# Optimization experiments

Hardware: AMD Instinct MI355X
Metric: run time of the kernel (lower is better)

## Reference

```python
import jax, jax.numpy as jnp
import numpy as np

N_LOW = 50000
N_HIGH = 200000
E = 1000000       # number of (i, j, k) triplets from the radius search
K = 27            # 3x3x3 voxel kernel cells
C_IN = 128
C_OUT = 128


def setup_inputs() -> dict:
    key = jax.random.key(0)
    k0, k1, k2, k3, k4, k5 = jax.random.split(key, 6)
    x_low = jax.random.normal(k0, (N_LOW, C_IN), dtype=jnp.float32)
    # PointConv3d weight: one [C_OUT, C_IN] matrix per kernel cell, kaiming-ish scale
    weight = jax.random.normal(k1, (K, C_OUT, C_IN), dtype=jnp.float32) * (1.0 / np.sqrt(C_IN))
    bias = jax.random.normal(k2, (C_OUT,), dtype=jnp.float32) * 0.01
    i_high = jax.random.randint(k3, (E,), 0, N_HIGH, dtype=jnp.int32)
    j_low = jax.random.randint(k4, (E,), 0, N_LOW, dtype=jnp.int32)
    k_cell = jax.random.randint(k5, (E,), 0, K, dtype=jnp.int32)
    return {"x_low": x_low, "weight": weight, "bias": bias,
            "i_high": i_high, "j_low": j_low, "k": k_cell, "n_high": N_HIGH}


def reference(x_low, weight, bias, i_high, j_low, k, n_high):
    # Sparse point convolution: out[i] += weight[k] @ x_low[j], then + bias.
    # Efficient form: transform every low-res point by all K kernel matrices once
    # (dense GEMM), then gather the (j, k) entry per triplet and scatter-add by i.
    y = jnp.einsum('nc,koc->nko', x_low, weight)       # [N_low, K, C_out]
    msg = y[j_low, k]                                  # [E, C_out] gather
    out = jnp.zeros((n_high, weight.shape[1]), dtype=x_low.dtype)
    out = out.at[i_high].add(msg)                      # scatter-add to high-res points
    return out + bias
```

## Files before the change

kernel.cpp:

```cpp
#include <hip/hip_runtime.h>

typedef _Float16 half8 __attribute__((ext_vector_type(8)));
typedef _Float16 half4v __attribute__((ext_vector_type(4)));
typedef _Float16 half2v __attribute__((ext_vector_type(2)));
typedef float f32x4 __attribute__((ext_vector_type(4)));

#define CAP 32
#define OVF_MAX 4096


__global__ void zero_ints(int* __restrict__ p, int n) {
    int i = blockIdx.x * blockDim.x + threadIdx.x;
    if (i < n) p[i] = 0;
}

__global__ void init_bias(float* __restrict__ out, const float* __restrict__ bias, int n4) {
    int i = blockIdx.x * blockDim.x + threadIdx.x;
    if (i >= n4) return;
    reinterpret_cast<float4*>(out)[i] = reinterpret_cast<const float4*>(bias)[i & 31];
}

__global__ __launch_bounds__(256) void cvt_mask(
    const float* __restrict__ x, const float* __restrict__ w,
    const float* __restrict__ bias,
    _Float16* __restrict__ Xh, _Float16* __restrict__ Wh,
    float* __restrict__ biasPerm, _Float16* __restrict__ Yz,
    const int* __restrict__ ih, const int* __restrict__ jl,
    const int* __restrict__ kc,
    unsigned char* __restrict__ maskB,
    int* __restrict__ counts, int* __restrict__ bucket,
    int* __restrict__ ovf_cnt, int* __restrict__ ovf_list,
    int Mpad, int ldY, int xv4, int xt4, int w4, int E, int eg) {
    int i = blockIdx.x * blockDim.x + threadIdx.x;
    if (i < xt4) {
        float4 v = (i < xv4) ? reinterpret_cast<const float4*>(x)[i]
                             : make_float4(0.f, 0.f, 0.f, 0.f);
        half4v h; h[0]=(_Float16)v.x; h[1]=(_Float16)v.y; h[2]=(_Float16)v.z; h[3]=(_Float16)v.w;
        reinterpret_cast<half4v*>(Xh)[i] = h;
    } else if (i < xt4 + w4) {
        int j = i - xt4;
        float4 v = reinterpret_cast<const float4*>(w)[j];
        half4v h; h[0]=(_Float16)v.x; h[1]=(_Float16)v.y; h[2]=(_Float16)v.z; h[3]=(_Float16)v.w;
        reinterpret_cast<half4v*>(Wh)[j] = h;
    } else if (i < xt4 + w4 + 32) {
        int j2 = i - xt4 - w4;
        int wn = j2 >> 4, mrow = j2 & 15;
        float4 v;
        v.x = bias[wn * 64 + 0 * 16 + mrow];
        v.y = bias[wn * 64 + 1 * 16 + mrow];
        v.z = bias[wn * 64 + 2 * 16 + mrow];
        v.w = bias[wn * 64 + 3 * 16 + mrow];
        reinterpret_cast<float4*>(biasPerm)[j2] = v;
    } else if (i < xt4 + w4 + 48) {
        int t = i - xt4 - w4 - 32;
        reinterpret_cast<int4*>(Yz)[t] = make_int4(0, 0, 0, 0);
    } else {
        int e = i - (xt4 + w4 + 48);
        if (e < E) {
            int j = jl[e], kk = kc[e];
            maskB[(size_t)kk * Mpad + j] = 1;
            if (e >= eg) {
                int ii = ih[e];
                int off = j * ldY + kk * 128;
                int pos = atomicAdd(&counts[ii], 1);
                if (pos < CAP) {
                    bucket[(size_t)ii * CAP + pos] = off;
                } else {
                    int o = atomicAdd(ovf_cnt, 1);
                    if (o < OVF_MAX) { ovf_list[2 * o] = ii; ovf_list[2 * o + 1] = off; }
                }
            }
        }
    }
}

__global__ __launch_bounds__(256) void gemm_xw(
    const _Float16* __restrict__ Xh,
    const _Float16* __restrict__ Wh,
    _Float16* __restrict__ Y,
    const unsigned char* __restrict__ maskB,
    _Float16* __restrict__ dump,
    int Mpad, int ldY, int KD,
    const int* __restrict__ ih, const int* __restrict__ jl,
    const int* __restrict__ kc,
    int* __restrict__ counts, int* __restrict__ bucket,
    int* __restrict__ ovf_cnt, int* __restrict__ ovf_list, int eg) {
    __shared__ ushort sA[128 * 128];
    __shared__ ushort sB[128 * 128];
    const int tid = threadIdx.x;

    const int nwg = gridDim.x;
    const int bid = blockIdx.x;
    {
    }
    const int q = nwg >> 3, r = nwg & 7;
    const int xcd = bid & 7, idx = bid >> 3;
    const int wg = (xcd < r) ? xcd * (q + 1) + idx
                             : r * (q + 1) + (xcd - r) * q + idx;
    const int mtile = wg / KD;
    const int ky = wg - mtile * KD;
    const int m0 = mtile * 128;
    const int kc0 = ky * 3;

    const int lane = tid & 63;
    const int wid = tid >> 6;
    const int wm = wid & 1, wn = wid >> 1;
    const int mrow = lane & 15;
    const int g = lane >> 4;

    const bool hasE = (bid * 256) < eg;
    int i0 = 0, off0 = 0, pos0 = CAP;
    if (hasE) {
        int e = bid * 256 + tid;
        i0 = ih[e];
        off0 = jl[e] * ldY + kc[e] * 128;
    }
    unsigned mwv0[4], mwv1[4], mwv2[4];
    {
        const unsigned char* mb = maskB + (size_t)kc0 * Mpad + m0 + wm * 64 + g * 4;
#pragma unroll
        for (int mt = 0; mt < 4; ++mt) {
            mwv0[mt] = *reinterpret_cast<const unsigned*>(mb + mt * 16);
            mwv1[mt] = *reinterpret_cast<const unsigned*>(mb + Mpad + mt * 16);
            mwv2[mt] = *reinterpret_cast<const unsigned*>(mb + 2 * Mpad + mt * 16);
        }
    }
    __builtin_amdgcn_sched_barrier(0);

    const ushort* Ag = (const ushort*)Xh + (size_t)m0 * 128;
#pragma unroll
    for (int it = 0; it < 8; ++it) {
        int p = it * 256 + tid;
        int row = p >> 4, cpos = p & 15;
        int csrc = cpos ^ (row & 15);
        __builtin_amdgcn_global_load_lds(
            (const __attribute__((address_space(1))) void*)(Ag + row * 128 + csrc * 8),
            (__attribute__((address_space(3))) void*)(&sA[row * 128 + cpos * 8]), 16, 0, 0);
    }
    {
        const ushort* Bg = (const ushort*)Wh + (size_t)kc0 * 128 * 128;
#pragma unroll
        for (int it = 0; it < 8; ++it) {
            int p = it * 256 + tid;
            int row = p >> 4, cpos = p & 15;
            int csrc = cpos ^ (row & 15);
            __builtin_amdgcn_global_load_lds(
                (const __attribute__((address_space(1))) void*)(Bg + row * 128 + csrc * 8),
                (__attribute__((address_space(3))) void*)(&sB[row * 128 + cpos * 8]), 16, 0, 0);
        }
    }
    __builtin_amdgcn_sched_barrier(0);

    if (hasE) {
        pos0 = atomicAdd(&counts[i0], 1);
        __builtin_amdgcn_sched_barrier(0);
        asm volatile("s_waitcnt vmcnt(1)" ::: "memory");
    } else {
        __builtin_amdgcn_sched_barrier(0);
        asm volatile("s_waitcnt vmcnt(0)" ::: "memory");
    }
    __builtin_amdgcn_sched_barrier(0);
    __builtin_amdgcn_s_barrier();
    __builtin_amdgcn_sched_barrier(0);

#pragma unroll
    for (int kk = 0; kk < 3; ++kk) {
        f32x4 acc[4][4] = {};
        __builtin_amdgcn_s_setprio(1);
#pragma unroll
        for (int kb = 0; kb < 4; ++kb) {
            half8 af[4], bf[4];
#pragma unroll
            for (int t = 0; t < 4; ++t) {
                int cpos8 = ((kb * 4 + g) ^ mrow) * 8;
                int ra = wm * 64 + t * 16 + mrow;
                af[t] = *reinterpret_cast<const half8*>(&sA[ra * 128 + cpos8]);
                int rb = wn * 64 + t * 16 + mrow;
                bf[t] = *reinterpret_cast<const half8*>(&sB[rb * 128 + cpos8]);
            }
#pragma unroll
            for (int mt = 0; mt < 4; ++mt)
#pragma unroll
                for (int nt = 0; nt < 4; ++nt)
                    acc[mt][nt] = __builtin_amdgcn_mfma_f32_16x16x32_f16(
                        af[mt], bf[nt], acc[mt][nt], 0, 0, 0);
        }
        __builtin_amdgcn_s_setprio(0);
        __builtin_amdgcn_sched_barrier(0);

        if (kk < 2) {
            __builtin_amdgcn_s_barrier();
            __builtin_amdgcn_sched_barrier(0);
            const ushort* Bg = (const ushort*)Wh + (size_t)(kc0 + kk + 1) * 128 * 128;
#pragma unroll
            for (int it = 0; it < 8; ++it) {
                int p = it * 256 + tid;
                int row = p >> 4, cpos = p & 15;
                int csrc = cpos ^ (row & 15);
                __builtin_amdgcn_global_load_lds(
                    (const __attribute__((address_space(1))) void*)(Bg + row * 128 + csrc * 8),
                    (__attribute__((address_space(3))) void*)(&sB[row * 128 + cpos * 8]), 16, 0, 0);
            }
            __builtin_amdgcn_sched_barrier(0);
        }
        if (kk == 0 && hasE) {
            if (pos0 < CAP) {
                bucket[(size_t)i0 * CAP + pos0] = off0;
            } else {
                int o = atomicAdd(ovf_cnt, 1);
                if (o < OVF_MAX) { ovf_list[2 * o] = i0; ovf_list[2 * o + 1] = off0; }
            }
        }
        _Float16* Yt = Y + (size_t)m0 * ldY + (kc0 + kk) * 128 + wn * 64 + mrow * 4;
        _Float16* dumpL = dump + lane * 4;
#pragma unroll
        for (int mt = 0; mt < 4; ++mt) {
            unsigned mw = (kk == 0) ? mwv0[mt] : (kk == 1) ? mwv1[mt] : mwv2[mt];
#pragma unroll
            for (int r = 0; r < 4; ++r) {
                int row = wm * 64 + mt * 16 + g * 4 + r;
                half4v hv;
#pragma unroll
                for (int nt = 0; nt < 4; ++nt) hv[nt] = (_Float16)acc[mt][nt][r];
                bool use = (mw >> (8 * r)) & 1u;
                _Float16* dst = use ? (Yt + (size_t)row * ldY) : dumpL;
                *reinterpret_cast<half4v*>(dst) = hv;
            }
        }
        __builtin_amdgcn_sched_barrier(0);
        if (kk == 0) {
            if (hasE) { asm volatile("s_waitcnt vmcnt(17)" ::: "memory"); }
            else      { asm volatile("s_waitcnt vmcnt(16)" ::: "memory"); }
            __builtin_amdgcn_sched_barrier(0);
            __builtin_amdgcn_s_barrier();
            __builtin_amdgcn_sched_barrier(0);
        } else if (kk == 1) {
            asm volatile("s_waitcnt vmcnt(16)" ::: "memory");
            __builtin_amdgcn_sched_barrier(0);
            __builtin_amdgcn_s_barrier();
            __builtin_amdgcn_sched_barrier(0);
        }
    }
}

__global__ __launch_bounds__(256) void gather_out(
    const _Float16* __restrict__ Y, const int* __restrict__ counts,
    const int* __restrict__ bucket, const float* __restrict__ biasPerm,
    float* __restrict__ out, int Nhigh, int zoff) {
    int wave = (blockIdx.x * blockDim.x + threadIdx.x) >> 6;
    int lane = threadIdx.x & 63;
    int p = lane >> 4;
    int sub = lane & 15;
    int i = wave * 4 + p;
    bool act = i < Nhigh;
    int iC = act ? i : 0;
    int nb = counts[iC];
    if (nb > CAP) nb = CAP;
    const int* bk = bucket + (size_t)iC * CAP;
    int offsA = bk[sub];
    int offsB = bk[sub + 16];
    float4 b0 = reinterpret_cast<const float4*>(biasPerm)[sub * 2];
    float4 b1 = reinterpret_cast<const float4*>(biasPerm)[sub * 2 + 1];
    float acc[8] = {b0.x, b0.y, b0.z, b0.w, b1.x, b1.y, b1.z, b1.w};

    int nmax = nb;
    nmax = max(nmax, __shfl_xor(nmax, 16));
    nmax = max(nmax, __shfl_xor(nmax, 32));

    for (int e0 = 0; e0 < nmax; e0 += 8) {
#pragma unroll
        for (int u = 0; u < 8; ++u) {
            int e = e0 + u;
            int off = (e < 16) ? __shfl(offsA, p * 16 + (e & 15))
                               : __shfl(offsB, p * 16 + (e & 15));
            bool valid = act && (e < nb);
            off = valid ? off : zoff;
            half8 h = *reinterpret_cast<const half8*>(Y + (size_t)off + sub * 8);
#pragma unroll
            for (int t = 0; t < 8; ++t) acc[t] += (float)h[t];
        }
    }
    if (act) {
        float* op = out + (size_t)i * 128;
        int obase = (sub >> 3) * 64 + (sub & 7) * 2;
#pragma unroll
        for (int t = 0; t < 8; ++t)
            op[obase + (t & 3) * 16 + (t >> 2)] = acc[t];
    }
}

__global__ void apply_overflow(const int* __restrict__ ovf_cnt, const int* __restrict__ ovf_list,
                               const _Float16* __restrict__ Y, float* __restrict__ out) {
    int n = *ovf_cnt;
    if (n > OVF_MAX) n = OVF_MAX;
    int lane = threadIdx.x & 63;
    int w = threadIdx.x >> 6;
    int o0p = 2 * lane, o1p = 2 * lane + 1;
    int o0 = (o0p >> 6) * 64 + (o0p & 3) * 16 + ((o0p >> 2) & 15);
    int o1 = (o1p >> 6) * 64 + (o1p & 3) * 16 + ((o1p >> 2) & 15);
    for (int o = w; o < n; o += 4) {
        int i = ovf_list[2 * o], off = ovf_list[2 * o + 1];
        half2v h = *reinterpret_cast<const half2v*>(Y + (size_t)off + lane * 2);
        float* dst = out + (size_t)i * 128;
        unsafeAtomicAdd(dst + o0, (float)h[0]);
        unsafeAtomicAdd(dst + o1, (float)h[1]);
    }
}

__global__ void fallback_edge(const float* __restrict__ x, const float* __restrict__ w,
                              const int* __restrict__ ih, const int* __restrict__ jl,
                              const int* __restrict__ kc, float* __restrict__ out, int E) {
    int e = blockIdx.x;
    if (e >= E) return;
    int lane = threadIdx.x;
    int i = ih[e], j = jl[e], k = kc[e];
    const float* xr = x + (size_t)j * 128;
    const float* wk = w + (size_t)k * 128 * 128;
    float s0 = 0.f, s1 = 0.f;
    for (int c = 0; c < 128; ++c) {
        float xv = xr[c];
        s0 += wk[(size_t)lane * 128 + c] * xv;
        s1 += wk[(size_t)(lane + 64) * 128 + c] * xv;
    }
    unsafeAtomicAdd(&out[(size_t)i * 128 + lane], s0);
    unsafeAtomicAdd(&out[(size_t)i * 128 + 64 + lane], s1);
}

extern "C" void kernel_launch(void* const* d_in, const int* in_sizes, int n_in,
                              void* d_out, int out_size, void* d_ws, size_t ws_size,
                              hipStream_t stream) {
    const float* x    = (const float*)d_in[0];
    const float* w    = (const float*)d_in[1];
    const float* bias = (const float*)d_in[2];
    const int*   ih   = (const int*)d_in[3];
    const int*   jl   = (const int*)d_in[4];
    const int*   kc   = (const int*)d_in[5];
    float* out = (float*)d_out;

    const int C = 128;
    const int Nlow = in_sizes[0] / C;
    const int K = in_sizes[1] / (C * C);
    const int E = in_sizes[3];
    const int ldY = K * C;
    const int Nhigh = out_size / C;

    const int mtiles = (Nlow + 127) / 128;
    const int Mpad = mtiles * 128;

    size_t off = 0;
    auto alloc = [&](size_t bytes) { size_t o = off; off = (off + bytes + 255) & ~(size_t)255; return o; };
    size_t xh_off   = alloc((size_t)Mpad * C * 2);
    size_t wh_off   = alloc((size_t)K * C * C * 2);
    size_t bp_off   = alloc((size_t)C * 4);
    size_t cnt_off  = alloc(((size_t)Nhigh + 1) * 4 + (size_t)Mpad * K);
    size_t ovl_off  = alloc((size_t)OVF_MAX * 2 * 4);
    size_t bkt_off  = alloc((size_t)Nhigh * CAP * 4);
    size_t dmp_off  = alloc(512);
    size_t y_off    = alloc(((size_t)Mpad * ldY + C) * 2);
    size_t need_sort = off;

    _Float16* Xh = (_Float16*)((char*)d_ws + xh_off);
    _Float16* Wh = (_Float16*)((char*)d_ws + wh_off);
    float* biasPerm = (float*)((char*)d_ws + bp_off);
    int* counts  = (int*)((char*)d_ws + cnt_off);
    int* ovf_cnt = counts + Nhigh;
    unsigned char* maskB = (unsigned char*)(counts + Nhigh + 1);
    int* ovf_lst = (int*)((char*)d_ws + ovl_off);
    int* bucket  = (int*)((char*)d_ws + bkt_off);
    _Float16* dump = (_Float16*)((char*)d_ws + dmp_off);
    _Float16* Y  = (_Float16*)((char*)d_ws + y_off);
    const int zoff = Mpad * ldY;

    if (ws_size >= need_sort && (K % 3) == 0) {
        int xv4 = Nlow * C / 4, xt4 = Mpad * C / 4;
        int w4 = K * C * C / 4;
        int KD = K / 3;
        int nwg = mtiles * KD;
        long long cap256 = (long long)nwg * 256;
        int eg = (E < cap256) ? (E & ~255) : (int)cap256;

        int nz = Nhigh + 1 + (Mpad * K) / 4;
        zero_ints<<<(nz + 255) / 256, 256, 0, stream>>>(counts, nz);

        int totalCvt = xt4 + w4 + 48 + E;
        cvt_mask<<<(totalCvt + 255) / 256, 256, 0, stream>>>(
            x, w, bias, Xh, Wh, biasPerm, Y + (size_t)zoff,
            ih, jl, kc, maskB, counts, bucket, ovf_cnt, ovf_lst,
            Mpad, ldY, xv4, xt4, w4, E, eg);

        gemm_xw<<<nwg, 256, 0, stream>>>(
            Xh, Wh, Y, maskB, dump, Mpad, ldY, KD,
            ih, jl, kc, counts, bucket, ovf_cnt, ovf_lst, eg);

        gather_out<<<(Nhigh + 15) / 16, 256, 0, stream>>>(
            Y, counts, bucket, biasPerm, out, Nhigh, zoff);
        apply_overflow<<<1, 256, 0, stream>>>(ovf_cnt, ovf_lst, Y, out);
    } else {
        int n4out = out_size / 4;
        init_bias<<<(n4out + 255) / 256, 256, 0, stream>>>(out, bias, n4out);
        fallback_edge<<<E, 64, 0, stream>>>(x, w, ih, jl, kc, out, E);
    }
}
```

Before: 357.2 us.

## Load GEMM B fragments directly from global into registers, drop LDS B tile

```diff
diff --git a/kernel.cpp b/kernel.cpp
--- a/kernel.cpp
+++ b/kernel.cpp
@@ -74,25 +74,21 @@
     }
 }
 
-__global__ __launch_bounds__(256) void gemm_xw(
+__global__ __launch_bounds__(256, 3) void gemm_xw(
     const _Float16* __restrict__ Xh,
     const _Float16* __restrict__ Wh,
     _Float16* __restrict__ Y,
     const unsigned char* __restrict__ maskB,
-    _Float16* __restrict__ dump,
     int Mpad, int ldY, int KD,
     const int* __restrict__ ih, const int* __restrict__ jl,
     const int* __restrict__ kc,
     int* __restrict__ counts, int* __restrict__ bucket,
     int* __restrict__ ovf_cnt, int* __restrict__ ovf_list, int eg) {
     __shared__ ushort sA[128 * 128];
-    __shared__ ushort sB[128 * 128];
     const int tid = threadIdx.x;
 
     const int nwg = gridDim.x;
     const int bid = blockIdx.x;
-    {
-    }
     const int q = nwg >> 3, r = nwg & 7;
     const int xcd = bid & 7, idx = bid >> 3;
     const int wg = (xcd < r) ? xcd * (q + 1) + idx
@@ -109,23 +105,30 @@
     const int g = lane >> 4;
 
     const bool hasE = (bid * 256) < eg;
-    int i0 = 0, off0 = 0, pos0 = CAP;
+    int ei = 0, ej = 0, ek = 0, pos0 = CAP;
     if (hasE) {
         int e = bid * 256 + tid;
-        i0 = ih[e];
-        off0 = jl[e] * ldY + kc[e] * 128;
-    }
-    unsigned mwv0[4], mwv1[4], mwv2[4];
+        ei = ih[e]; ej = jl[e]; ek = kc[e];
+    }
+
+    unsigned mwv[3][4];
     {
         const unsigned char* mb = maskB + (size_t)kc0 * Mpad + m0 + wm * 64 + g * 4;
 #pragma unroll
-        for (int mt = 0; mt < 4; ++mt) {
-            mwv0[mt] = *reinterpret_cast<const unsigned*>(mb + mt * 16);
-            mwv1[mt] = *reinterpret_cast<const unsigned*>(mb + Mpad + mt * 16);
-            mwv2[mt] = *reinterpret_cast<const unsigned*>(mb + 2 * Mpad + mt * 16);
-        }
-    }
-    __builtin_amdgcn_sched_barrier(0);
+        for (int kkq = 0; kkq < 3; ++kkq)
+#pragma unroll
+            for (int mt = 0; mt < 4; ++mt)
+                mwv[kkq][mt] = *reinterpret_cast<const unsigned*>(mb + kkq * Mpad + mt * 16);
+    }
+
+    const int rbBase = wn * 64 + mrow;
+    half8 bf[2][4];
+    {
+        const ushort* B0 = (const ushort*)Wh + (size_t)kc0 * 16384;
+#pragma unroll
+        for (int t = 0; t < 4; ++t)
+            bf[0][t] = *reinterpret_cast<const half8*>(B0 + (rbBase + t * 16) * 128 + g * 8);
+    }
 
     const ushort* Ag = (const ushort*)Xh + (size_t)m0 * 128;
 #pragma unroll
@@ -137,22 +140,12 @@
             (const __attribute__((address_space(1))) void*)(Ag + row * 128 + csrc * 8),
             (__attribute__((address_space(3))) void*)(&sA[row * 128 + cpos * 8]), 16, 0, 0);
     }
-    {
-        const ushort* Bg = (const ushort*)Wh + (size_t)kc0 * 128 * 128;
-#pragma unroll
-        for (int it = 0; it < 8; ++it) {
-            int p = it * 256 + tid;
-            int row = p >> 4, cpos = p & 15;
-            int csrc = cpos ^ (row & 15);
-            __builtin_amdgcn_global_load_lds(
-                (const __attribute__((address_space(1))) void*)(Bg + row * 128 + csrc * 8),
-                (__attribute__((address_space(3))) void*)(&sB[row * 128 + cpos * 8]), 16, 0, 0);
-        }
-    }
     __builtin_amdgcn_sched_barrier(0);
 
+    int off0 = 0;
     if (hasE) {
-        pos0 = atomicAdd(&counts[i0], 1);
+        off0 = ej * ldY + ek * 128;
+        pos0 = atomicAdd(&counts[ei], 1);
         __builtin_amdgcn_sched_barrier(0);
         asm volatile("s_waitcnt vmcnt(1)" ::: "memory");
     } else {
@@ -166,79 +159,54 @@
 #pragma unroll
     for (int kk = 0; kk < 3; ++kk) {
         f32x4 acc[4][4] = {};
-        __builtin_amdgcn_s_setprio(1);
 #pragma unroll
         for (int kb = 0; kb < 4; ++kb) {
-            half8 af[4], bf[4];
-#pragma unroll
-            for (int t = 0; t < 4; ++t) {
-                int cpos8 = ((kb * 4 + g) ^ mrow) * 8;
-                int ra = wm * 64 + t * 16 + mrow;
-                af[t] = *reinterpret_cast<const half8*>(&sA[ra * 128 + cpos8]);
-                int rb = wn * 64 + t * 16 + mrow;
-                bf[t] = *reinterpret_cast<const half8*>(&sB[rb * 128 + cpos8]);
+            const int cur = kb & 1, nxt = cur ^ 1;
+            if (!(kk == 2 && kb == 3)) {
+                const int nkk = (kb < 3) ? kk : kk + 1;
+                const int nkb = (kb < 3) ? kb + 1 : 0;
+                const ushort* Bn = (const ushort*)Wh + (size_t)(kc0 + nkk) * 16384;
+#pragma unroll
+                for (int t = 0; t < 4; ++t)
+                    bf[nxt][t] = *reinterpret_cast<const half8*>(
+                        Bn + (rbBase + t * 16) * 128 + (nkb * 4 + g) * 8);
             }
+            half8 af[4];
+            const int cpos8 = ((kb * 4 + g) ^ mrow) * 8;
+#pragma unroll
+            for (int t = 0; t < 4; ++t)
+                af[t] = *reinterpret_cast<const half8*>(
+                    &sA[(wm * 64 + t * 16 + mrow) * 128 + cpos8]);
 #pragma unroll
             for (int mt = 0; mt < 4; ++mt)
 #pragma unroll
                 for (int nt = 0; nt < 4; ++nt)
                     acc[mt][nt] = __builtin_amdgcn_mfma_f32_16x16x32_f16(
-                        af[mt], bf[nt], acc[mt][nt], 0, 0, 0);
-        }
-        __builtin_amdgcn_s_setprio(0);
-        __builtin_amdgcn_sched_barrier(0);
-
-        if (kk < 2) {
-            __builtin_amdgcn_s_barrier();
-            __builtin_amdgcn_sched_barrier(0);
-            const ushort* Bg = (const ushort*)Wh + (size_t)(kc0 + kk + 1) * 128 * 128;
-#pragma unroll
-            for (int it = 0; it < 8; ++it) {
-                int p = it * 256 + tid;
-                int row = p >> 4, cpos = p & 15;
-                int csrc = cpos ^ (row & 15);
-                __builtin_amdgcn_global_load_lds(
-                    (const __attribute__((address_space(1))) void*)(Bg + row * 128 + csrc * 8),
-                    (__attribute__((address_space(3))) void*)(&sB[row * 128 + cpos * 8]), 16, 0, 0);
-            }
-            __builtin_amdgcn_sched_barrier(0);
-        }
+                        af[mt], bf[cur][nt], acc[mt][nt], 0, 0, 0);
+        }
+
         if (kk == 0 && hasE) {
             if (pos0 < CAP) {
-                bucket[(size_t)i0 * CAP + pos0] = off0;
+                bucket[(size_t)ei * CAP + pos0] = off0;
             } else {
                 int o = atomicAdd(ovf_cnt, 1);
-                if (o < OVF_MAX) { ovf_list[2 * o] = i0; ovf_list[2 * o + 1] = off0; }
+                if (o < OVF_MAX) { ovf_list[2 * o] = ei; ovf_list[2 * o + 1] = off0; }
             }
         }
         _Float16* Yt = Y + (size_t)m0 * ldY + (kc0 + kk) * 128 + wn * 64 + mrow * 4;
-        _Float16* dumpL = dump + lane * 4;
 #pragma unroll
         for (int mt = 0; mt < 4; ++mt) {
-            unsigned mw = (kk == 0) ? mwv0[mt] : (kk == 1) ? mwv1[mt] : mwv2[mt];
+            unsigned mw = mwv[kk][mt];
 #pragma unroll
             for (int r = 0; r < 4; ++r) {
-                int row = wm * 64 + mt * 16 + g * 4 + r;
-                half4v hv;
-#pragma unroll
-                for (int nt = 0; nt < 4; ++nt) hv[nt] = (_Float16)acc[mt][nt][r];
-                bool use = (mw >> (8 * r)) & 1u;
-                _Float16* dst = use ? (Yt + (size_t)row * ldY) : dumpL;
-                *reinterpret_cast<half4v*>(dst) = hv;
+                if ((mw >> (8 * r)) & 1u) {
+                    int row = wm * 64 + mt * 16 + g * 4 + r;
+                    half4v hv;
+#pragma unroll
+                    for (int nt = 0; nt < 4; ++nt) hv[nt] = (_Float16)acc[mt][nt][r];
+                    *reinterpret_cast<half4v*>(Yt + (size_t)row * ldY) = hv;
+                }
             }
-        }
-        __builtin_amdgcn_sched_barrier(0);
-        if (kk == 0) {
-            if (hasE) { asm volatile("s_waitcnt vmcnt(17)" ::: "memory"); }
-            else      { asm volatile("s_waitcnt vmcnt(16)" ::: "memory"); }
-            __builtin_amdgcn_sched_barrier(0);
-            __builtin_amdgcn_s_barrier();
-            __builtin_amdgcn_sched_barrier(0);
-        } else if (kk == 1) {
-            asm volatile("s_waitcnt vmcnt(16)" ::: "memory");
-            __builtin_amdgcn_sched_barrier(0);
-            __builtin_amdgcn_s_barrier();
-            __builtin_amdgcn_sched_barrier(0);
         }
     }
 }
@@ -355,7 +323,6 @@
     size_t cnt_off  = alloc(((size_t)Nhigh + 1) * 4 + (size_t)Mpad * K);
     size_t ovl_off  = alloc((size_t)OVF_MAX * 2 * 4);
     size_t bkt_off  = alloc((size_t)Nhigh * CAP * 4);
-    size_t dmp_off  = alloc(512);
     size_t y_off    = alloc(((size_t)Mpad * ldY + C) * 2);
     size_t need_sort = off;
 
@@ -367,7 +334,6 @@
     unsigned char* maskB = (unsigned char*)(counts + Nhigh + 1);
     int* ovf_lst = (int*)((char*)d_ws + ovl_off);
     int* bucket  = (int*)((char*)d_ws + bkt_off);
-    _Float16* dump = (_Float16*)((char*)d_ws + dmp_off);
     _Float16* Y  = (_Float16*)((char*)d_ws + y_off);
     const int zoff = Mpad * ldY;
 
@@ -389,7 +355,7 @@
             Mpad, ldY, xv4, xt4, w4, E, eg);
 
         gemm_xw<<<nwg, 256, 0, stream>>>(
-            Xh, Wh, Y, maskB, dump, Mpad, ldY, KD,
+            Xh, Wh, Y, maskB, Mpad, ldY, KD,
             ih, jl, kc, counts, bucket, ovf_cnt, ovf_lst, eg);
 
         gather_out<<<(Nhigh + 15) / 16, 256, 0, stream>>>(
```

After: 420.8 us. +17.8%, slower.

## Branch-skip masked Y stores, load masks lazily, use nontemporal stores

Applied to the files above, without the earlier changes.

```diff
diff --git a/kernel.cpp b/kernel.cpp
--- a/kernel.cpp
+++ b/kernel.cpp
@@ -4,6 +4,7 @@
 typedef _Float16 half4v __attribute__((ext_vector_type(4)));
 typedef _Float16 half2v __attribute__((ext_vector_type(2)));
 typedef float f32x4 __attribute__((ext_vector_type(4)));
+typedef float f32x2 __attribute__((ext_vector_type(2)));
 
 #define CAP 32
 #define OVF_MAX 4096
@@ -79,7 +80,6 @@
     const _Float16* __restrict__ Wh,
     _Float16* __restrict__ Y,
     const unsigned char* __restrict__ maskB,
-    _Float16* __restrict__ dump,
     int Mpad, int ldY, int KD,
     const int* __restrict__ ih, const int* __restrict__ jl,
     const int* __restrict__ kc,
@@ -91,8 +91,6 @@
 
     const int nwg = gridDim.x;
     const int bid = blockIdx.x;
-    {
-    }
     const int q = nwg >> 3, r = nwg & 7;
     const int xcd = bid & 7, idx = bid >> 3;
     const int wg = (xcd < r) ? xcd * (q + 1) + idx
@@ -102,31 +100,6 @@
     const int m0 = mtile * 128;
     const int kc0 = ky * 3;
 
-    const int lane = tid & 63;
-    const int wid = tid >> 6;
-    const int wm = wid & 1, wn = wid >> 1;
-    const int mrow = lane & 15;
-    const int g = lane >> 4;
-
-    const bool hasE = (bid * 256) < eg;
-    int i0 = 0, off0 = 0, pos0 = CAP;
-    if (hasE) {
-        int e = bid * 256 + tid;
-        i0 = ih[e];
-        off0 = jl[e] * ldY + kc[e] * 128;
-    }
-    unsigned mwv0[4], mwv1[4], mwv2[4];
-    {
-        const unsigned char* mb = maskB + (size_t)kc0 * Mpad + m0 + wm * 64 + g * 4;
-#pragma unroll
-        for (int mt = 0; mt < 4; ++mt) {
-            mwv0[mt] = *reinterpret_cast<const unsigned*>(mb + mt * 16);
-            mwv1[mt] = *reinterpret_cast<const unsigned*>(mb + Mpad + mt * 16);
-            mwv2[mt] = *reinterpret_cast<const unsigned*>(mb + 2 * Mpad + mt * 16);
-        }
-    }
-    __builtin_amdgcn_sched_barrier(0);
-
     const ushort* Ag = (const ushort*)Xh + (size_t)m0 * 128;
 #pragma unroll
     for (int it = 0; it < 8; ++it) {
@@ -151,10 +124,15 @@
     }
     __builtin_amdgcn_sched_barrier(0);
 
+    const bool hasE = (bid * 256) < eg;
+    int i0 = 0, off0 = 0, pos0 = CAP;
     if (hasE) {
+        int e = bid * 256 + tid;
+        i0 = ih[e];
+        off0 = jl[e] * ldY + kc[e] * 128;
         pos0 = atomicAdd(&counts[i0], 1);
         __builtin_amdgcn_sched_barrier(0);
-        asm volatile("s_waitcnt vmcnt(1)" ::: "memory");
+        asm volatile("s_waitcnt vmcnt(4)" ::: "memory");
     } else {
         __builtin_amdgcn_sched_barrier(0);
         asm volatile("s_waitcnt vmcnt(0)" ::: "memory");
@@ -163,10 +141,14 @@
     __builtin_amdgcn_s_barrier();
     __builtin_amdgcn_sched_barrier(0);
 
-#pragma unroll
+    const int lane = tid & 63;
+    const int wid = tid >> 6;
+    const int wm = wid & 1, wn = wid >> 1;
+    const int mrow = lane & 15;
+    const int g = lane >> 4;
+
     for (int kk = 0; kk < 3; ++kk) {
         f32x4 acc[4][4] = {};
-        __builtin_amdgcn_s_setprio(1);
 #pragma unroll
         for (int kb = 0; kb < 4; ++kb) {
             half8 af[4], bf[4];
@@ -185,9 +167,6 @@
                     acc[mt][nt] = __builtin_amdgcn_mfma_f32_16x16x32_f16(
                         af[mt], bf[nt], acc[mt][nt], 0, 0, 0);
         }
-        __builtin_amdgcn_s_setprio(0);
-        __builtin_amdgcn_sched_barrier(0);
-
         if (kk < 2) {
             __builtin_amdgcn_s_barrier();
             __builtin_amdgcn_sched_barrier(0);
@@ -211,20 +190,23 @@
                 if (o < OVF_MAX) { ovf_list[2 * o] = i0; ovf_list[2 * o + 1] = off0; }
             }
         }
+        const unsigned char* mBp = maskB + (size_t)(kc0 + kk) * Mpad + m0 + wm * 64;
         _Float16* Yt = Y + (size_t)m0 * ldY + (kc0 + kk) * 128 + wn * 64 + mrow * 4;
-        _Float16* dumpL = dump + lane * 4;
 #pragma unroll
         for (int mt = 0; mt < 4; ++mt) {
-            unsigned mw = (kk == 0) ? mwv0[mt] : (kk == 1) ? mwv1[mt] : mwv2[mt];
-#pragma unroll
-            for (int r = 0; r < 4; ++r) {
-                int row = wm * 64 + mt * 16 + g * 4 + r;
-                half4v hv;
-#pragma unroll
-                for (int nt = 0; nt < 4; ++nt) hv[nt] = (_Float16)acc[mt][nt][r];
-                bool use = (mw >> (8 * r)) & 1u;
-                _Float16* dst = use ? (Yt + (size_t)row * ldY) : dumpL;
-                *reinterpret_cast<half4v*>(dst) = hv;
+            unsigned mw = *reinterpret_cast<const unsigned*>(mBp + mt * 16 + g * 4);
+            if (mw) {
+#pragma unroll
+                for (int r = 0; r < 4; ++r) {
+                    if ((mw >> (8 * r)) & 0xFFu) {
+                        int row = wm * 64 + mt * 16 + g * 4 + r;
+                        half4v hv;
+#pragma unroll
+                        for (int nt = 0; nt < 4; ++nt) hv[nt] = (_Float16)acc[mt][nt][r];
+                        __builtin_nontemporal_store(
+                            hv, reinterpret_cast<half4v*>(Yt + (size_t)row * ldY));
+                    }
+                }
             }
         }
         __builtin_amdgcn_sched_barrier(0);
@@ -284,8 +266,11 @@
         float* op = out + (size_t)i * 128;
         int obase = (sub >> 3) * 64 + (sub & 7) * 2;
 #pragma unroll
-        for (int t = 0; t < 8; ++t)
-            op[obase + (t & 3) * 16 + (t >> 2)] = acc[t];
+        for (int b = 0; b < 4; ++b) {
+            f32x2 v; v[0] = acc[b]; v[1] = acc[b + 4];
+            __builtin_nontemporal_store(
+                v, reinterpret_cast<f32x2*>(op + obase + 16 * b));
+        }
     }
 }
 
@@ -355,7 +340,6 @@
     size_t cnt_off  = alloc(((size_t)Nhigh + 1) * 4 + (size_t)Mpad * K);
     size_t ovl_off  = alloc((size_t)OVF_MAX * 2 * 4);
     size_t bkt_off  = alloc((size_t)Nhigh * CAP * 4);
-    size_t dmp_off  = alloc(512);
     size_t y_off    = alloc(((size_t)Mpad * ldY + C) * 2);
     size_t need_sort = off;
 
@@ -367,7 +351,6 @@
     unsigned char* maskB = (unsigned char*)(counts + Nhigh + 1);
     int* ovf_lst = (int*)((char*)d_ws + ovl_off);
     int* bucket  = (int*)((char*)d_ws + bkt_off);
-    _Float16* dump = (_Float16*)((char*)d_ws + dmp_off);
     _Float16* Y  = (_Float16*)((char*)d_ws + y_off);
     const int zoff = Mpad * ldY;
 
@@ -389,7 +372,7 @@
             Mpad, ldY, xv4, xt4, w4, E, eg);
 
         gemm_xw<<<nwg, 256, 0, stream>>>(
-            Xh, Wh, Y, maskB, dump, Mpad, ldY, KD,
+            Xh, Wh, Y, maskB, Mpad, ldY, KD,
             ih, jl, kc, counts, bucket, ovf_cnt, ovf_lst, eg);
 
         gather_out<<<(Nhigh + 15) / 16, 256, 0, stream>>>(
```

Measured after the change: 326.8 us. 1.09x faster.
